# Performance work log

Hardware: AMD Instinct MI355X
Metric: run time of the kernel (lower is better)

Reference implementation:

```python
import jax, jax.numpy as jnp
import numpy as np

SIGMA = 10.0
GAMMA = 1.0 / (2.0 * SIGMA ** 2)


def setup_inputs() -> dict:
    key = jax.random.key(0)
    k1, k2 = jax.random.split(key)
    x1 = jax.random.normal(k1, (8192, 128), dtype=jnp.float32)
    x2 = jax.random.normal(k2, (8192, 128), dtype=jnp.float32)
    return {"x1": x1, "x2": x2}


def reference(x1, x2):
    # ||x1_i - x2_j||^2 = ||x1_i||^2 - 2 x1_i.x2_j + ||x2_j||^2
    # (same math as diag(x@x.T), computed as row sums-of-squares)
    n1 = jnp.sum(x1 * x1, axis=-1, keepdims=True)        # [n1, 1]
    n2 = jnp.sum(x2 * x2, axis=-1, keepdims=True).T      # [1, n2]
    cross = x1 @ x2.T                                    # [n1, n2]
    norm_sq = n1 - 2.0 * cross + n2
    return jnp.exp(-GAMMA * norm_sq)
```

## Files before the change

### kernel.cpp

```cpp
#include <hip/hip_runtime.h>
#include <stdint.h>


#define GAMMA_F 0.005f

typedef __attribute__((ext_vector_type(8))) _Float16 half8;
typedef __attribute__((ext_vector_type(2))) _Float16 half2v;
typedef __attribute__((ext_vector_type(4))) float floatx4;

__device__ __forceinline__ void async_copy16(const void* g, void* l) {
    __builtin_amdgcn_global_load_lds(
        (const __attribute__((address_space(1))) void*)g,
        (__attribute__((address_space(3))) void*)l,
        16, 0, 0);
}

__global__ __launch_bounds__(256) void rbf_prep(
    const float* __restrict__ x1, const float* __restrict__ x2,
    _Float16* __restrict__ Ah, _Float16* __restrict__ Bh,
    float* __restrict__ n1, float* __restrict__ n2) {
    const int wave = threadIdx.x >> 6;
    const int lane = threadIdx.x & 63;
    const int row = blockIdx.x * 4 + wave;
    const float* src; _Float16* dst; float* nrm; int r;
    if (row < 8192) { src = x1; dst = Ah; nrm = n1; r = row; }
    else            { src = x2; dst = Bh; nrm = n2; r = row - 8192; }
    const float2 v = ((const float2*)(src + (size_t)r * 128))[lane];
    float s = v.x * v.x + v.y * v.y;
    half2v h;
    h.x = (_Float16)v.x;
    h.y = (_Float16)v.y;
    ((half2v*)(dst + (size_t)r * 128))[lane] = h;
    #pragma unroll
    for (int off = 32; off > 0; off >>= 1) s += __shfl_down(s, off, 64);
    if (lane == 0) nrm[r] = s;
}

__global__ __launch_bounds__(256, 2) void rbf_main(
    const _Float16* __restrict__ A,
    const _Float16* __restrict__ B,
    const float* __restrict__ n1, const float* __restrict__ n2,
    float* __restrict__ out) {
    __shared__ alignas(16) _Float16 As[128 * 128];
    __shared__ alignas(16) _Float16 Bs[128 * 128];

    const int t  = threadIdx.x;
    const int tm = blockIdx.x >> 6;
    const int tn = blockIdx.x & 63;

    const char* Ag = (const char*)(A + (size_t)tm * 128 * 128);
    const char* Bg = (const char*)(B + (size_t)tn * 128 * 128);
    char* AsB = (char*)As;
    char* BsB = (char*)Bs;

    #pragma unroll
    for (int i = 0; i < 8; ++i) {
        const int p = i * 256 + t;
        const int m = p >> 4;
        const int c = (p & 15) ^ (m & 15);
        const int goff = m * 256 + c * 16;
        async_copy16(Ag + goff, AsB + p * 16);
        async_copy16(Bg + goff, BsB + p * 16);
    }
    __syncthreads();

    const int lane   = t & 63;
    const int wave   = t >> 6;
    const int ln     = lane & 15;
    const int q      = lane >> 4;
    const int wave_m = (wave & 1) * 64;
    const int wave_n = (wave >> 1) * 64;

    floatx4 acc[4][4] = {};

    #pragma unroll
    for (int ks = 0; ks < 4; ++ks) {
        const int xk = ((4 * ks + q) ^ ln) * 16;
        half8 a_frag[4], b_frag[4];
        #pragma unroll
        for (int i = 0; i < 4; ++i) {
            a_frag[i] = *(const half8*)(AsB + (wave_m + i * 16 + ln) * 256 + xk);
            b_frag[i] = *(const half8*)(BsB + (wave_n + i * 16 + ln) * 256 + xk);
        }
        #pragma unroll
        for (int i = 0; i < 4; ++i)
            #pragma unroll
            for (int j = 0; j < 4; ++j)
                acc[i][j] = __builtin_amdgcn_mfma_f32_16x16x32_f16(
                    a_frag[i], b_frag[j], acc[i][j], 0, 0, 0);
    }

    const int row0 = tm * 128 + wave_m;
    const int col0 = tn * 128 + wave_n + ln;
    float n2v[4];
    #pragma unroll
    for (int j = 0; j < 4; ++j) n2v[j] = n2[col0 + j * 16];

    #pragma unroll
    for (int i = 0; i < 4; ++i) {
        const int r0 = row0 + i * 16 + q * 4;
        const float4 nv = *(const float4*)(n1 + r0);
        const float n1v[4] = {nv.x, nv.y, nv.z, nv.w};
        #pragma unroll
        for (int r = 0; r < 4; ++r) {
            float* orow = out + (size_t)(r0 + r) * 8192 + col0;
            #pragma unroll
            for (int j = 0; j < 4; ++j) {
                const float s = n1v[r] + n2v[j] - 2.0f * acc[i][j][r];
                orow[j * 16] = __expf(-GAMMA_F * s);
            }
        }
    }
}

extern "C" void kernel_launch(void* const* d_in, const int* in_sizes, int n_in,
                              void* d_out, int out_size, void* d_ws, size_t ws_size,
                              hipStream_t stream) {
    const float* x1 = (const float*)d_in[0];
    const float* x2 = (const float*)d_in[1];
    float* out = (float*)d_out;

    char* ws = (char*)d_ws;
    _Float16* Ah = (_Float16*)ws;
    _Float16* Bh = (_Float16*)(ws + (size_t)2 * 1024 * 1024);
    float* n1 = (float*)(ws + (size_t)4 * 1024 * 1024);
    float* n2 = (float*)(ws + (size_t)4 * 1024 * 1024 + 32 * 1024);

    rbf_prep<<<4096, 256, 0, stream>>>(x1, x2, Ah, Bh, n1, n2);
    rbf_main<<<4096, 256, 0, stream>>>(Ah, Bh, n1, n2, out);
}
```

Baseline: 274.6 us.

## Transpose MFMA operands for float4 output stores and fold gamma into exp2

Swaps the A and B operands of the MFMA so each lane's four accumulator values lie along the output row. The epilogue can then write float4 vectors instead of scalar stores. The norms are pre-scaled by -gamma*log2(e) in the prep kernel, so the exponent becomes one fma plus a raw exp2. This aims to cut store instruction count and write inefficiency on the 256MB output, with slightly different rounding in the exponent.

New measurement: 274.6 us. Within noise of the previous version (-0.0%).

```diff
diff --git a/kernel.cpp b/kernel.cpp
--- a/kernel.cpp
+++ b/kernel.cpp
@@ -2,7 +2,8 @@
 #include <stdint.h>
 
 
-#define GAMMA_F 0.005f
+#define CL_F     0.0072134752f
+#define TWO_CL_F 0.0144269504f
 
 typedef __attribute__((ext_vector_type(8))) _Float16 half8;
 typedef __attribute__((ext_vector_type(2))) _Float16 half2v;
@@ -33,7 +34,7 @@
     ((half2v*)(dst + (size_t)r * 128))[lane] = h;
     #pragma unroll
     for (int off = 32; off > 0; off >>= 1) s += __shfl_down(s, off, 64);
-    if (lane == 0) nrm[r] = s;
+    if (lane == 0) nrm[r] = -CL_F * s;
 }
 
 __global__ __launch_bounds__(256, 2) void rbf_main(
@@ -87,28 +88,31 @@
             #pragma unroll
             for (int j = 0; j < 4; ++j)
                 acc[i][j] = __builtin_amdgcn_mfma_f32_16x16x32_f16(
-                    a_frag[i], b_frag[j], acc[i][j], 0, 0, 0);
+                    b_frag[j], a_frag[i], acc[i][j], 0, 0, 0);
     }
 
-    const int row0 = tm * 128 + wave_m;
-    const int col0 = tn * 128 + wave_n + ln;
-    float n2v[4];
+    const int row0 = tm * 128 + wave_m + ln;
+    const int colb = tn * 128 + wave_n + q * 4;
+
+    float n1s[4];
     #pragma unroll
-    for (int j = 0; j < 4; ++j) n2v[j] = n2[col0 + j * 16];
+    for (int i = 0; i < 4; ++i) n1s[i] = n1[row0 + i * 16];
+
+    float4 n2s[4];
+    #pragma unroll
+    for (int j = 0; j < 4; ++j) n2s[j] = *(const float4*)(n2 + colb + j * 16);
 
     #pragma unroll
     for (int i = 0; i < 4; ++i) {
-        const int r0 = row0 + i * 16 + q * 4;
-        const float4 nv = *(const float4*)(n1 + r0);
-        const float n1v[4] = {nv.x, nv.y, nv.z, nv.w};
+        float* orow = out + (size_t)(row0 + i * 16) * 8192 + colb;
         #pragma unroll
-        for (int r = 0; r < 4; ++r) {
-            float* orow = out + (size_t)(r0 + r) * 8192 + col0;
-            #pragma unroll
-            for (int j = 0; j < 4; ++j) {
-                const float s = n1v[r] + n2v[j] - 2.0f * acc[i][j][r];
-                orow[j * 16] = __expf(-GAMMA_F * s);
-            }
+        for (int j = 0; j < 4; ++j) {
+            float4 o;
+            o.x = __builtin_amdgcn_exp2f(fmaf(acc[i][j][0], TWO_CL_F, n1s[i] + n2s[j].x));
+            o.y = __builtin_amdgcn_exp2f(fmaf(acc[i][j][1], TWO_CL_F, n1s[i] + n2s[j].y));
+            o.z = __builtin_amdgcn_exp2f(fmaf(acc[i][j][2], TWO_CL_F, n1s[i] + n2s[j].z));
+            o.w = __builtin_amdgcn_exp2f(fmaf(acc[i][j][3], TWO_CL_F, n1s[i] + n2s[j].w));
+            *(float4*)(orow + j * 16) = o;
         }
     }
 }
```
